# Kernel tuning notes

Measured on AMD Instinct MI355X. Metric: run time of the kernel, lower is better.

The kernel has to match this reference:

```python
import jax, jax.numpy as jnp
from jax import lax
import numpy as np

B, S, D_IN = 2048, 512, 5
H, E_DIM, N_EMB, C_CONV = 64, 32, 64, 32
COMMIT = 0.01


def _lstm_params(key, in_dim, hid):
    ks = jax.random.split(key, 4)
    sc = 1.0 / np.sqrt(hid)
    wih = jax.random.uniform(ks[0], (4 * hid, in_dim), minval=-sc, maxval=sc)
    whh = jax.random.uniform(ks[1], (4 * hid, hid), minval=-sc, maxval=sc)
    bih = jax.random.uniform(ks[2], (4 * hid,), minval=-sc, maxval=sc)
    bhh = jax.random.uniform(ks[3], (4 * hid,), minval=-sc, maxval=sc)
    return wih, whh, bih, bhh


def setup_inputs() -> dict:
    key = jax.random.key(0)
    ks = jax.random.split(key, 12)
    inp = {}
    inp['x'] = jax.random.normal(ks[0], (B, S, D_IN), dtype=jnp.float32)
    inp['conv_w'] = jax.random.normal(ks[1], (C_CONV, D_IN, 3)) * 0.2  # OIH
    inp['conv_b'] = jax.random.normal(ks[2], (C_CONV,)) * 0.05
    inp['bn_g'] = jnp.ones((C_CONV,)) + jax.random.normal(ks[3], (C_CONV,)) * 0.05
    inp['bn_b'] = jax.random.normal(ks[4], (C_CONV,)) * 0.05
    inp['bn_m'] = jax.random.normal(ks[5], (C_CONV,)) * 0.1
    inp['bn_v'] = jax.random.uniform(ks[6], (C_CONV,), minval=0.5, maxval=1.5)
    cw = _lstm_params(ks[7], C_CONV, H)
    cw1 = _lstm_params(jax.random.fold_in(ks[7], 1), H, H)
    vw = _lstm_params(ks[8], D_IN, H)
    vw1 = _lstm_params(jax.random.fold_in(ks[8], 1), H, H)
    for pre, p in (('cnn0', cw), ('cnn1', cw1), ('vq0', vw), ('vq1', vw1)):
        inp[pre + '_wih'], inp[pre + '_whh'], inp[pre + '_bih'], inp[pre + '_bhh'] = p
    inp['proj_w'] = jax.random.normal(ks[9], (E_DIM, H)) * (1.0 / np.sqrt(H))
    inp['proj_b'] = jax.random.normal(ks[10], (E_DIM,)) * 0.05
    xav = np.sqrt(6.0 / (N_EMB + E_DIM))
    inp['codebook'] = jax.random.uniform(ks[11], (N_EMB, E_DIM), minval=-xav, maxval=xav)
    return inp


def _lstm_layer(xs, wih, whh, bih, bhh):
    # xs: [S, B, in] -> (ys [S,B,H], h_final [B,H])
    b = xs.shape[1]
    h0 = jnp.zeros((b, H), xs.dtype)
    bias = bih + bhh

    def step(carry, x_t):
        h, c = carry
        gates = x_t @ wih.T + h @ whh.T + bias
        i, f, g, o = jnp.split(gates, 4, axis=-1)
        c = jax.nn.sigmoid(f) * c + jax.nn.sigmoid(i) * jnp.tanh(g)
        h = jax.nn.sigmoid(o) * jnp.tanh(c)
        return (h, c), h

    (h, c), ys = lax.scan(step, (h0, h0), xs)
    return ys, h


def _forward(x, conv_w, conv_b, bn_g, bn_b, bn_m, bn_v,
             cnn0_wih, cnn0_whh, cnn0_bih, cnn0_bhh,
             cnn1_wih, cnn1_whh, cnn1_bih, cnn1_bhh,
             vq0_wih, vq0_whh, vq0_bih, vq0_bhh,
             vq1_wih, vq1_whh, vq1_bih, vq1_bhh,
             proj_w, proj_b, codebook):
    # CNN stream: conv1d(k=3, pad=1) + BN (eval) + ReLU; dropout = identity (eval)
    x_ncw = jnp.transpose(x, (0, 2, 1))  # [B, D_IN, S]
    y = lax.conv_general_dilated(x_ncw, conv_w, (1,), [(1, 1)],
                                 dimension_numbers=('NCH', 'OIH', 'NCH'))
    y = y + conv_b[None, :, None]
    y = (y - bn_m[None, :, None]) * (bn_g / jnp.sqrt(bn_v + 1e-5))[None, :, None] + bn_b[None, :, None]
    y = jax.nn.relu(y)
    y = jnp.transpose(y, (2, 0, 1))  # [S, B, 32] time-major
    ys, _ = _lstm_layer(y, cnn0_wih, cnn0_whh, cnn0_bih, cnn0_bhh)
    _, cnn_features = _lstm_layer(ys, cnn1_wih, cnn1_whh, cnn1_bih, cnn1_bhh)  # [B, H]

    # VQ stream
    xt = jnp.transpose(x, (1, 0, 2))  # [S, B, D_IN]
    ys2, _ = _lstm_layer(xt, vq0_wih, vq0_whh, vq0_bih, vq0_bhh)
    _, vq_hidden = _lstm_layer(ys2, vq1_wih, vq1_whh, vq1_bih, vq1_bhh)  # [B, H]
    vq_proj = vq_hidden @ proj_w.T + proj_b  # [B, E_DIM]

    # Vector quantization
    d = (jnp.sum(vq_proj ** 2, axis=1, keepdims=True)
         + jnp.sum(codebook ** 2, axis=1)
         - 2.0 * vq_proj @ codebook.T)  # [B, N_EMB]
    idx = jnp.argmin(d, axis=1)
    quantized = codebook[idx]  # [B, E_DIM]
    e_loss = jnp.mean((lax.stop_gradient(quantized) - vq_proj) ** 2)
    q_loss = jnp.mean((quantized - lax.stop_gradient(vq_proj)) ** 2)
    vq_loss = q_loss + COMMIT * e_loss
    quantized = vq_proj + lax.stop_gradient(quantized - vq_proj)  # STE
    enc = jax.nn.one_hot(idx, N_EMB, dtype=vq_proj.dtype)
    avg_probs = jnp.mean(enc, axis=0)
    perplexity = jnp.exp(-jnp.sum(avg_probs * jnp.log(avg_probs + 1e-10)))

    combined = jnp.concatenate([cnn_features, quantized], axis=1)  # [B, H+E_DIM]
    return combined, vq_loss, perplexity


def reference(x, conv_w, conv_b, bn_g, bn_b, bn_m, bn_v,
              cnn0_wih, cnn0_whh, cnn0_bih, cnn0_bhh,
              cnn1_wih, cnn1_whh, cnn1_bih, cnn1_bhh,
              vq0_wih, vq0_whh, vq0_bih, vq0_bhh,
              vq1_wih, vq1_whh, vq1_bih, vq1_bhh,
              proj_w, proj_b, codebook):
    combined, vq_loss, perplexity = _forward(
        x, conv_w, conv_b, bn_g, bn_b, bn_m, bn_v,
        cnn0_wih, cnn0_whh, cnn0_bih, cnn0_bhh,
        cnn1_wih, cnn1_whh, cnn1_bih, cnn1_bhh,
        vq0_wih, vq0_whh, vq0_bih, vq0_bhh,
        vq1_wih, vq1_whh, vq1_bih, vq1_bhh,
        proj_w, proj_b, codebook)
    # num_classes=None -> returns (combined, combined, vq_loss, perplexity)
    return combined, combined, vq_loss, perplexity
```

## Files before the change

kernel.cpp:

```cpp
#include <hip/hip_runtime.h>
#include <math.h>
#include <stdint.h>

#define B_TOT 2048
#define SEQ   512
#define DIN   5
#define HID   64
#define EDIM  32
#define NEMB  64
#define BT    16
#define NBLK_STREAM 128
#define COMB  96
#define OUTC  (B_TOT*COMB)

typedef __attribute__((ext_vector_type(8))) _Float16 half8;
typedef __attribute__((ext_vector_type(4))) float float4v;

#if __has_builtin(__builtin_amdgcn_exp2f)
#define FEXP2(x) __builtin_amdgcn_exp2f(x)
#else
#define FEXP2(x) exp2f(x)
#endif
#if __has_builtin(__builtin_amdgcn_rcpf)
#define FRCP(x) __builtin_amdgcn_rcpf(x)
#else
#define FRCP(x) (1.0f/(x))
#endif

__device__ __forceinline__ float fsig(float x){
  return FRCP(1.0f + FEXP2(-1.44269504089f * x));
}
__device__ __forceinline__ float ftanh(float x){
  return fmaf(2.0f, FRCP(1.0f + FEXP2(-2.88539008178f * x)), -1.0f);
}
#define MFMA16(a,b,c) __builtin_amdgcn_mfma_f32_16x16x32_f16((a),(b),(c),0,0,0)

__global__ __launch_bounds__(1024)
__attribute__((amdgpu_waves_per_eu(4, 4)))
void fused_kernel(const float* __restrict__ xg,
                  const float* __restrict__ conv_w, const float* __restrict__ conv_b,
                  const float* __restrict__ bn_g, const float* __restrict__ bn_b,
                  const float* __restrict__ bn_m, const float* __restrict__ bn_v,
                  const float* __restrict__ cnn0_wih, const float* __restrict__ cnn0_whh,
                  const float* __restrict__ cnn0_bih, const float* __restrict__ cnn0_bhh,
                  const float* __restrict__ cnn1_wih, const float* __restrict__ cnn1_whh,
                  const float* __restrict__ cnn1_bih, const float* __restrict__ cnn1_bhh,
                  const float* __restrict__ vq0_wih, const float* __restrict__ vq0_whh,
                  const float* __restrict__ vq0_bih, const float* __restrict__ vq0_bhh,
                  const float* __restrict__ vq1_wih, const float* __restrict__ vq1_whh,
                  const float* __restrict__ vq1_bih, const float* __restrict__ vq1_bhh,
                  const float* __restrict__ proj_w, const float* __restrict__ proj_b,
                  const float* __restrict__ codebook,
                  float* __restrict__ out, float* __restrict__ ws_f,
                  int* __restrict__ ws_hist)
{
  __shared__ __align__(16) _Float16 ZT[2][5][4][BT][8];
  __shared__ __align__(16) float hfin[BT][HID];
  __shared__ __align__(16) float pbuf[BT][EDIM];
  __shared__ float xwin[4][BT][DIN];

  const int tid  = threadIdx.x;
  const bool is_cnn = (blockIdx.x < NBLK_STREAM);
  const int b0   = (is_cnn ? blockIdx.x : blockIdx.x - NBLK_STREAM) * BT;
  const int w    = tid >> 6;
  const int lane = tid & 63;
  const int n16  = lane & 15;
  const int quad = lane >> 4;
  const int u    = 4*w + quad;

  const float* wih0 = is_cnn ? cnn0_wih : vq0_wih;
  const float* whh0 = is_cnn ? cnn0_whh : vq0_whh;
  const float* bih0 = is_cnn ? cnn0_bih : vq0_bih;
  const float* bhh0 = is_cnn ? cnn0_bhh : vq0_bhh;
  const float* wih1 = is_cnn ? cnn1_wih : vq1_wih;
  const float* whh1 = is_cnn ? cnn1_whh : vq1_whh;
  const float* bih1 = is_cnn ? cnn1_bih : vq1_bih;
  const float* bhh1 = is_cnn ? cnn1_bhh : vq1_bhh;

  const int orow = 64*(n16 & 3) + 4*w + (n16 >> 2);
  half8 Ah0[3], Ah1[4];
#pragma unroll
  for (int kt = 0; kt < 3; ++kt) {
    half8 vh;
#pragma unroll
    for (int j = 0; j < 8; ++j) {
      const int g = kt*32 + quad*8 + j;
      float wv;
      if (is_cnn) wv = (g < 32) ? wih0[orow*32 + g] : whh0[orow*64 + (g-32)];
      else        wv = (g < 5) ? wih0[orow*5 + g] : (g < 32 ? 0.f : whh0[orow*64 + (g-32)]);
      vh[j] = (_Float16)wv;
    }
    Ah0[kt] = vh;
  }
#pragma unroll
  for (int kt = 0; kt < 4; ++kt) {
    half8 vh;
#pragma unroll
    for (int j = 0; j < 8; ++j) {
      const int g = kt*32 + quad*8 + j;
      float wv = (g < 64) ? wih1[orow*64 + g] : whh1[orow*64 + (g-64)];
      vh[j] = (_Float16)wv;
    }
    Ah1[kt] = vh;
  }

  float4v bc0, bc1;
#pragma unroll
  for (int r = 0; r < 4; ++r) {
    bc0[r] = bih0[64*r + u] + bhh0[64*r + u];
    bc1[r] = bih1[64*r + u] + bhh1[64*r + u];
  }

  float wr[16];
#pragma unroll
  for (int i = 0; i < 16; ++i) wr[i] = 0.f;
  if (is_cnn && tid < 512) {
    const int cc = tid >> 4;
    float s = bn_g[cc] * rsqrtf(bn_v[cc] + 1e-5f);
#pragma unroll
    for (int i = 0; i < 5; ++i)
#pragma unroll
      for (int tau = 0; tau < 3; ++tau)
        wr[tau*5 + i] = conv_w[cc*15 + i*3 + tau] * s;
    wr[15] = (conv_b[cc] - bn_m[cc]) * s + bn_b[cc];
  }

  for (int i2 = tid; i2 < 2*5*4*BT*8/2; i2 += 1024) ((uint32_t*)ZT)[i2] = 0;

  const int xn = tid / 5, xi = tid % 5;
  float xpref = 0.f;

  #define ZB(b) ((_Float16*)(&ZT[(b)][0][0][0][0]))
  #define ZIDX(tile,k32,n) (((tile)*4 + (((k32)>>3)&3))*(BT*8) + (n)*8 + ((k32)&7))

  if (is_cnn) {
    if (tid < BT*DIN) {
#pragma unroll
      for (int j = 0; j < 4; ++j)
        xwin[j][xn][xi] = xg[((size_t)(b0+xn)*SEQ + j)*DIN + xi];
    }
    __syncthreads();
    if (tid < 512) {
      const int cc = tid >> 4, cn = tid & 15;
      float s = wr[15];
#pragma unroll
      for (int i = 0; i < 5; ++i)
        s += wr[5+i]*xwin[0][cn][i] + wr[10+i]*xwin[1][cn][i];
      s = fmaxf(s, 0.f);
      ZB(1)[ZIDX(0, cc, cn)] = (_Float16)s;
    }
  } else {
    if (tid < BT*DIN) {
      float xv = xg[((size_t)(b0+xn)*SEQ + 0)*DIN + xi];
      ZB(1)[ZIDX(0, xi, xn)] = (_Float16)xv;
    }
  }
  __syncthreads();

  float c0 = 0.f, c1 = 0.f, h1v = 0.f;
  {
    half8 bt0 = *(const half8*)&ZT[1][0][quad][n16][0];
    half8 bt1 = *(const half8*)&ZT[1][1][quad][n16][0];
    half8 bt2 = *(const half8*)&ZT[1][2][quad][n16][0];
    float4v a0 = bc0;
    a0 = MFMA16(Ah0[0], bt0, a0);
    a0 = MFMA16(Ah0[1], bt1, a0);
    a0 = MFMA16(Ah0[2], bt2, a0);
    c0 = fsig(a0[1])*c0 + fsig(a0[0])*ftanh(a0[2]);
    float h0 = fsig(a0[3])*ftanh(c0);
    ZB(0)[ZIDX(1 + (u>>5), u & 31, n16)] = (_Float16)h0;
  }
  if (is_cnn) {
    if (tid < 512) {
      const int cc = tid >> 4, cn = tid & 15;
      float s = wr[15];
#pragma unroll
      for (int i = 0; i < 5; ++i)
        s += wr[i]*xwin[0][cn][i] + wr[5+i]*xwin[1][cn][i]
           + wr[10+i]*xwin[2][cn][i];
      s = fmaxf(s, 0.f);
      ZB(0)[ZIDX(0, cc, cn)] = (_Float16)s;
    }
    if (tid < BT*DIN) xpref = xg[((size_t)(b0+xn)*SEQ + 4)*DIN + xi];
  } else {
    if (tid < BT*DIN) {
      float xv = xg[((size_t)(b0+xn)*SEQ + 1)*DIN + xi];
      ZB(0)[ZIDX(0, xi, xn)] = (_Float16)xv;
      xpref = xg[((size_t)(b0+xn)*SEQ + 2)*DIN + xi];
    }
  }
  __syncthreads();

#pragma unroll 2
  for (int t = 0; t < SEQ; ++t) {
    const int rb = t & 1, wrb = rb ^ 1;
    half8 bt0 = *(const half8*)&ZT[rb][0][quad][n16][0];
    half8 bt1 = *(const half8*)&ZT[rb][1][quad][n16][0];
    half8 bt2 = *(const half8*)&ZT[rb][2][quad][n16][0];
    half8 bt3 = *(const half8*)&ZT[rb][3][quad][n16][0];
    half8 bt4 = *(const half8*)&ZT[rb][4][quad][n16][0];
    float4v a1 = bc1, a0 = bc0;
    a1 = MFMA16(Ah1[0], bt1, a1);
    a1 = MFMA16(Ah1[1], bt2, a1);
    a1 = MFMA16(Ah1[2], bt3, a1);
    a1 = MFMA16(Ah1[3], bt4, a1);
    a0 = MFMA16(Ah0[0], bt0, a0);
    a0 = MFMA16(Ah0[1], bt1, a0);
    a0 = MFMA16(Ah0[2], bt2, a0);

    {
      c1 = fsig(a1[1])*c1 + fsig(a1[0])*ftanh(a1[2]);
      float h1 = fsig(a1[3])*ftanh(c1);
      ZB(wrb)[ZIDX(3 + (u>>5), u & 31, n16)] = (_Float16)h1;
      if (is_cnn) h1v = h1;
      else if (t == SEQ-1) hfin[n16][u] = h1;
    }
    {
      c0 = fsig(a0[1])*c0 + fsig(a0[0])*ftanh(a0[2]);
      float h0 = fsig(a0[3])*ftanh(c0);
      ZB(wrb)[ZIDX(1 + (u>>5), u & 31, n16)] = (_Float16)h0;
    }
    if (is_cnn) {
      if (tid < 512) {
        const int cc = tid >> 4, cn = tid & 15;
        const int s1 = (t+1)&3, s2 = (t+2)&3, s3 = (t+3)&3;
        float s = wr[15];
#pragma unroll
        for (int i = 0; i < 5; ++i)
          s += wr[i]*xwin[s1][cn][i] + wr[5+i]*xwin[s2][cn][i]
             + wr[10+i]*xwin[s3][cn][i];
        s = fmaxf(s, 0.f);
        ZB(wrb)[ZIDX(0, cc, cn)] = (_Float16)s;
      }
      if (tid < BT*DIN) {
        xwin[t & 3][xn][xi] = xpref;
        const int tq = t + 5;
        xpref = (tq < SEQ) ? xg[((size_t)(b0+xn)*SEQ + tq)*DIN + xi] : 0.f;
      }
    } else {
      if (tid < BT*DIN) {
        ZB(wrb)[ZIDX(0, xi, xn)] = (_Float16)xpref;
        const int tq = t + 3;
        xpref = (tq < SEQ) ? xg[((size_t)(b0+xn)*SEQ + tq)*DIN + xi] : 0.f;
      }
    }
    __syncthreads();
  }

  if (is_cnn) {
    const size_t gb = (size_t)(b0 + n16);
    out[gb*COMB + u]        = h1v;
    out[OUTC + gb*COMB + u] = h1v;
  } else {
    if (tid < 512) {
      const int pn = tid >> 5, pe = tid & 31;
      float s = proj_b[pe];
      const float* pw = proj_w + pe*HID;
#pragma unroll
      for (int k = 0; k < HID; ++k) s += hfin[pn][k] * pw[k];
      pbuf[pn][pe] = s;
    }
    __syncthreads();
    {
      const int bb = w;
      const int nn = lane;
      const float* cbn = codebook + nn*EDIM;
      float d = 0.f;
#pragma unroll
      for (int k = 0; k < EDIM; ++k) { float df = pbuf[bb][k] - cbn[k]; d += df*df; }
      int bi = nn;
#pragma unroll
      for (int off = 32; off > 0; off >>= 1) {
        float od = __shfl_down(d, off, 64);
        int   oi = __shfl_down(bi, off, 64);
        if (od < d || (od == d && oi < bi)) { d = od; bi = oi; }
      }
      bi = __shfl(bi, 0, 64);
      float lv = 0.f;
      if (nn < EDIM) {
        float q = codebook[bi*EDIM + nn];
        const size_t gb = (size_t)(b0 + bb);
        out[gb*COMB + HID + nn]        = q;
        out[OUTC + gb*COMB + HID + nn] = q;
        float df = q - pbuf[bb][nn];
        lv = df*df;
      }
#pragma unroll
      for (int off = 32; off > 0; off >>= 1) lv += __shfl_down(lv, off, 64);
      if (nn == 0) { atomicAdd(ws_f, lv); atomicAdd(&ws_hist[bi], 1); }
    }
  }
}

__global__ void zero_ws_kernel(float* ws_f, int* ws_hist) {
  const int t = threadIdx.x;
  if (t == 0) ws_f[0] = 0.f;
  if (t < NEMB) ws_hist[t] = 0;
}

__global__ void vq_finalize_kernel(const float* __restrict__ ws_f,
                                   const int* __restrict__ ws_hist,
                                   float* __restrict__ out) {
  const int t = threadIdx.x;
  float p = (float)ws_hist[t] * (1.0f / (float)B_TOT);
  float e = -p * logf(p + 1e-10f);
#pragma unroll
  for (int off = 32; off > 0; off >>= 1) e += __shfl_down(e, off, 64);
  if (t == 0) {
    float mse = ws_f[0] * (1.0f / (float)(B_TOT * EDIM));
    out[2*OUTC + 0] = mse * 1.01f;
    out[2*OUTC + 1] = expf(e);
  }
}

extern "C" void kernel_launch(void* const* d_in, const int* in_sizes, int n_in,
                              void* d_out, int out_size, void* d_ws, size_t ws_size,
                              hipStream_t stream) {
  const float* x        = (const float*)d_in[0];
  const float* conv_w   = (const float*)d_in[1];
  const float* conv_b   = (const float*)d_in[2];
  const float* bn_g     = (const float*)d_in[3];
  const float* bn_b     = (const float*)d_in[4];
  const float* bn_m     = (const float*)d_in[5];
  const float* bn_v     = (const float*)d_in[6];
  const float* cnn0_wih = (const float*)d_in[7];
  const float* cnn0_whh = (const float*)d_in[8];
  const float* cnn0_bih = (const float*)d_in[9];
  const float* cnn0_bhh = (const float*)d_in[10];
  const float* cnn1_wih = (const float*)d_in[11];
  const float* cnn1_whh = (const float*)d_in[12];
  const float* cnn1_bih = (const float*)d_in[13];
  const float* cnn1_bhh = (const float*)d_in[14];
  const float* vq0_wih  = (const float*)d_in[15];
  const float* vq0_whh  = (const float*)d_in[16];
  const float* vq0_bih  = (const float*)d_in[17];
  const float* vq0_bhh  = (const float*)d_in[18];
  const float* vq1_wih  = (const float*)d_in[19];
  const float* vq1_whh  = (const float*)d_in[20];
  const float* vq1_bih  = (const float*)d_in[21];
  const float* vq1_bhh  = (const float*)d_in[22];
  const float* proj_w   = (const float*)d_in[23];
  const float* proj_b   = (const float*)d_in[24];
  const float* codebook = (const float*)d_in[25];

  float* out     = (float*)d_out;
  float* ws_f    = (float*)d_ws;
  int*   ws_hist = (int*)d_ws + 16;

  hipLaunchKernelGGL(zero_ws_kernel, dim3(1), dim3(64), 0, stream, ws_f, ws_hist);
  hipLaunchKernelGGL(fused_kernel, dim3(2*NBLK_STREAM), dim3(1024), 0, stream,
                     x, conv_w, conv_b, bn_g, bn_b, bn_m, bn_v,
                     cnn0_wih, cnn0_whh, cnn0_bih, cnn0_bhh,
                     cnn1_wih, cnn1_whh, cnn1_bih, cnn1_bhh,
                     vq0_wih, vq0_whh, vq0_bih, vq0_bhh,
                     vq1_wih, vq1_whh, vq1_bih, vq1_bhh,
                     proj_w, proj_b, codebook, out, ws_f, ws_hist);
  hipLaunchKernelGGL(vq_finalize_kernel, dim3(1), dim3(64), 0, stream, ws_f, ws_hist, out);
}
```

Measured before the change: 559.4 us.

## Precompute conv+BN+ReLU features into workspace and stream them into the LSTM loop

Adds a separate kernel that computes the folded conv/BN/ReLU features for all timesteps as fp16 into workspace. The CNN-stream LSTM blocks then load these prefetched half8 vectors instead of computing the convolution inside the serial time loop. The loop barrier is also replaced with an explicit lgkmcnt wait plus s_barrier. This takes per-step ALU work off the recurrent critical path, at the cost of an extra launch and about 64MB of global traffic. The new path is only taken when the workspace is large enough.

```diff
diff --git a/kernel.cpp b/kernel.cpp
--- a/kernel.cpp
+++ b/kernel.cpp
@@ -35,6 +35,57 @@
 }
 #define MFMA16(a,b,c) __builtin_amdgcn_mfma_f32_16x16x32_f16((a),(b),(c),0,0,0)
 
+#define LOOP_BARRIER() do { \
+    asm volatile("s_waitcnt lgkmcnt(0)" ::: "memory"); \
+    __builtin_amdgcn_s_barrier(); \
+  } while (0)
+
+__global__ __launch_bounds__(256)
+void conv_pre_kernel(const float* __restrict__ xg,
+                     const float* __restrict__ conv_w, const float* __restrict__ conv_b,
+                     const float* __restrict__ bn_g, const float* __restrict__ bn_b,
+                     const float* __restrict__ bn_m, const float* __restrict__ bn_v,
+                     _Float16* __restrict__ Y)
+{
+  __shared__ float wcs[16][32];
+  const int tid = threadIdx.x;
+  if (tid < 32) {
+    float s = bn_g[tid] * rsqrtf(bn_v[tid] + 1e-5f);
+#pragma unroll
+    for (int i = 0; i < 5; ++i)
+#pragma unroll
+      for (int tau = 0; tau < 3; ++tau)
+        wcs[tau*5 + i][tid] = conv_w[tid*15 + i*3 + tau] * s;
+    wcs[15][tid] = (conv_b[tid] - bn_m[tid]) * s + bn_b[tid];
+  }
+  __syncthreads();
+  const int total = B_TOT * SEQ;
+  for (int idx = blockIdx.x*256 + tid; idx < total; idx += gridDim.x*256) {
+    const int b = idx >> 9, t = idx & (SEQ-1);
+    const float* xb = xg + ((size_t)b*SEQ + t)*DIN;
+    float xm[5], x0[5], xp[5];
+#pragma unroll
+    for (int i = 0; i < 5; ++i) {
+      x0[i] = xb[i];
+      xm[i] = (t > 0)       ? xb[i - DIN] : 0.f;
+      xp[i] = (t < SEQ-1)   ? xb[i + DIN] : 0.f;
+    }
+    _Float16 yv[32];
+#pragma unroll
+    for (int ch = 0; ch < 32; ++ch) {
+      float s = wcs[15][ch];
+#pragma unroll
+      for (int i = 0; i < 5; ++i)
+        s += wcs[i][ch]*xm[i] + wcs[5+i][ch]*x0[i] + wcs[10+i][ch]*xp[i];
+      yv[ch] = (_Float16)fmaxf(s, 0.f);
+    }
+    half8* dst = (half8*)(Y + (size_t)idx*32);
+#pragma unroll
+    for (int g = 0; g < 4; ++g) dst[g] = *(half8*)&yv[g*8];
+  }
+}
+
+template<bool PRE>
 __global__ __launch_bounds__(1024)
 __attribute__((amdgpu_waves_per_eu(4, 4)))
 void fused_kernel(const float* __restrict__ xg,
@@ -50,7 +101,7 @@
                   const float* __restrict__ vq1_wih, const float* __restrict__ vq1_whh,
                   const float* __restrict__ vq1_bih, const float* __restrict__ vq1_bhh,
                   const float* __restrict__ proj_w, const float* __restrict__ proj_b,
-                  const float* __restrict__ codebook,
+                  const float* __restrict__ codebook, const _Float16* __restrict__ Yg,
                   float* __restrict__ out, float* __restrict__ ws_f,
                   int* __restrict__ ws_hist)
 {
@@ -112,47 +163,70 @@
   }
 
   float wr[16];
-#pragma unroll
-  for (int i = 0; i < 16; ++i) wr[i] = 0.f;
-  if (is_cnn && tid < 512) {
-    const int cc = tid >> 4;
-    float s = bn_g[cc] * rsqrtf(bn_v[cc] + 1e-5f);
-#pragma unroll
-    for (int i = 0; i < 5; ++i)
-#pragma unroll
-      for (int tau = 0; tau < 3; ++tau)
-        wr[tau*5 + i] = conv_w[cc*15 + i*3 + tau] * s;
-    wr[15] = (conv_b[cc] - bn_m[cc]) * s + bn_b[cc];
+  if (!PRE) {
+#pragma unroll
+    for (int i = 0; i < 16; ++i) wr[i] = 0.f;
+    if (is_cnn && tid < 512) {
+      const int cc = tid >> 4;
+      float s = bn_g[cc] * rsqrtf(bn_v[cc] + 1e-5f);
+#pragma unroll
+      for (int i = 0; i < 5; ++i)
+#pragma unroll
+        for (int tau = 0; tau < 3; ++tau)
+          wr[tau*5 + i] = conv_w[cc*15 + i*3 + tau] * s;
+      wr[15] = (conv_b[cc] - bn_m[cc]) * s + bn_b[cc];
+    }
   }
 
   for (int i2 = tid; i2 < 2*5*4*BT*8/2; i2 += 1024) ((uint32_t*)ZT)[i2] = 0;
 
   const int xn = tid / 5, xi = tid % 5;
+  const int yn = tid >> 2, ykg = tid & 3;
   float xpref = 0.f;
+  half8 ypref{};
+  const _Float16* Yb = nullptr;
+  if (PRE && is_cnn && tid < 64)
+    Yb = Yg + ((size_t)(b0 + yn)*SEQ)*32 + ykg*8;
 
   #define ZB(b) ((_Float16*)(&ZT[(b)][0][0][0][0]))
   #define ZIDX(tile,k32,n) (((tile)*4 + (((k32)>>3)&3))*(BT*8) + (n)*8 + ((k32)&7))
 
-  if (is_cnn) {
+  if (!PRE && is_cnn) {
     if (tid < BT*DIN) {
 #pragma unroll
       for (int j = 0; j < 4; ++j)
         xwin[j][xn][xi] = xg[((size_t)(b0+xn)*SEQ + j)*DIN + xi];
     }
-    __syncthreads();
-    if (tid < 512) {
-      const int cc = tid >> 4, cn = tid & 15;
-      float s = wr[15];
-#pragma unroll
-      for (int i = 0; i < 5; ++i)
-        s += wr[5+i]*xwin[0][cn][i] + wr[10+i]*xwin[1][cn][i];
-      s = fmaxf(s, 0.f);
-      ZB(1)[ZIDX(0, cc, cn)] = (_Float16)s;
+  }
+  __syncthreads();
+
+  if (is_cnn) {
+    if (PRE) {
+      if (tid < 64) {
+        half8 y0 = *(const half8*)(Yb + (size_t)0*32);
+        half8 y1 = *(const half8*)(Yb + (size_t)1*32);
+        ypref    = *(const half8*)(Yb + (size_t)2*32);
+        *(half8*)&ZB(1)[ykg*(BT*8) + yn*8] = y0;
+        *(half8*)&ZB(0)[ykg*(BT*8) + yn*8] = y1;
+      }
+    } else {
+      if (tid < 512) {
+        const int cc = tid >> 4, cn = tid & 15;
+        float s = wr[15];
+#pragma unroll
+        for (int i = 0; i < 5; ++i)
+          s += wr[5+i]*xwin[0][cn][i] + wr[10+i]*xwin[1][cn][i];
+        s = fmaxf(s, 0.f);
+        ZB(1)[ZIDX(0, cc, cn)] = (_Float16)s;
+      }
     }
   } else {
     if (tid < BT*DIN) {
-      float xv = xg[((size_t)(b0+xn)*SEQ + 0)*DIN + xi];
-      ZB(1)[ZIDX(0, xi, xn)] = (_Float16)xv;
+      float x0v = xg[((size_t)(b0+xn)*SEQ + 0)*DIN + xi];
+      float x1v = xg[((size_t)(b0+xn)*SEQ + 1)*DIN + xi];
+      ZB(1)[ZIDX(0, xi, xn)] = (_Float16)x0v;
+      ZB(0)[ZIDX(0, xi, xn)] = (_Float16)x1v;
+      xpref = xg[((size_t)(b0+xn)*SEQ + 2)*DIN + xi];
     }
   }
   __syncthreads();
@@ -170,7 +244,7 @@
     float h0 = fsig(a0[3])*ftanh(c0);
     ZB(0)[ZIDX(1 + (u>>5), u & 31, n16)] = (_Float16)h0;
   }
-  if (is_cnn) {
+  if (!PRE && is_cnn) {
     if (tid < 512) {
       const int cc = tid >> 4, cn = tid & 15;
       float s = wr[15];
@@ -182,12 +256,6 @@
       ZB(0)[ZIDX(0, cc, cn)] = (_Float16)s;
     }
     if (tid < BT*DIN) xpref = xg[((size_t)(b0+xn)*SEQ + 4)*DIN + xi];
-  } else {
-    if (tid < BT*DIN) {
-      float xv = xg[((size_t)(b0+xn)*SEQ + 1)*DIN + xi];
-      ZB(0)[ZIDX(0, xi, xn)] = (_Float16)xv;
-      xpref = xg[((size_t)(b0+xn)*SEQ + 2)*DIN + xi];
-    }
   }
   __syncthreads();
 
@@ -221,21 +289,29 @@
       ZB(wrb)[ZIDX(1 + (u>>5), u & 31, n16)] = (_Float16)h0;
     }
     if (is_cnn) {
-      if (tid < 512) {
-        const int cc = tid >> 4, cn = tid & 15;
-        const int s1 = (t+1)&3, s2 = (t+2)&3, s3 = (t+3)&3;
-        float s = wr[15];
-#pragma unroll
-        for (int i = 0; i < 5; ++i)
-          s += wr[i]*xwin[s1][cn][i] + wr[5+i]*xwin[s2][cn][i]
-             + wr[10+i]*xwin[s3][cn][i];
-        s = fmaxf(s, 0.f);
-        ZB(wrb)[ZIDX(0, cc, cn)] = (_Float16)s;
-      }
-      if (tid < BT*DIN) {
-        xwin[t & 3][xn][xi] = xpref;
-        const int tq = t + 5;
-        xpref = (tq < SEQ) ? xg[((size_t)(b0+xn)*SEQ + tq)*DIN + xi] : 0.f;
+      if (PRE) {
+        if (tid < 64) {
+          *(half8*)&ZB(wrb)[ykg*(BT*8) + yn*8] = ypref;
+          const int tq = t + 3;
+          if (tq < SEQ) ypref = *(const half8*)(Yb + (size_t)tq*32);
+        }
+      } else {
+        if (tid < 512) {
+          const int cc = tid >> 4, cn = tid & 15;
+          const int s1 = (t+1)&3, s2 = (t+2)&3, s3 = (t+3)&3;
+          float s = wr[15];
+#pragma unroll
+          for (int i = 0; i < 5; ++i)
+            s += wr[i]*xwin[s1][cn][i] + wr[5+i]*xwin[s2][cn][i]
+               + wr[10+i]*xwin[s3][cn][i];
+          s = fmaxf(s, 0.f);
+          ZB(wrb)[ZIDX(0, cc, cn)] = (_Float16)s;
+        }
+        if (tid < BT*DIN) {
+          xwin[t & 3][xn][xi] = xpref;
+          const int tq = t + 5;
+          xpref = (tq < SEQ) ? xg[((size_t)(b0+xn)*SEQ + tq)*DIN + xi] : 0.f;
+        }
       }
     } else {
       if (tid < BT*DIN) {
@@ -244,7 +320,7 @@
         xpref = (tq < SEQ) ? xg[((size_t)(b0+xn)*SEQ + tq)*DIN + xi] : 0.f;
       }
     }
-    __syncthreads();
+    LOOP_BARRIER();
   }
 
   if (is_cnn) {
@@ -347,13 +423,29 @@
   float* ws_f    = (float*)d_ws;
   int*   ws_hist = (int*)d_ws + 16;
 
+  const size_t Y_BYTES = (size_t)B_TOT * SEQ * 32 * sizeof(_Float16);
+  _Float16* Yg = (_Float16*)((char*)d_ws + 1024);
+  const bool use_pre = (ws_size >= 1024 + Y_BYTES);
+
   hipLaunchKernelGGL(zero_ws_kernel, dim3(1), dim3(64), 0, stream, ws_f, ws_hist);
-  hipLaunchKernelGGL(fused_kernel, dim3(2*NBLK_STREAM), dim3(1024), 0, stream,
-                     x, conv_w, conv_b, bn_g, bn_b, bn_m, bn_v,
-                     cnn0_wih, cnn0_whh, cnn0_bih, cnn0_bhh,
-                     cnn1_wih, cnn1_whh, cnn1_bih, cnn1_bhh,
-                     vq0_wih, vq0_whh, vq0_bih, vq0_bhh,
-                     vq1_wih, vq1_whh, vq1_bih, vq1_bhh,
-                     proj_w, proj_b, codebook, out, ws_f, ws_hist);
+  if (use_pre) {
+    hipLaunchKernelGGL(conv_pre_kernel, dim3(1024), dim3(256), 0, stream,
+                       x, conv_w, conv_b, bn_g, bn_b, bn_m, bn_v, Yg);
+    hipLaunchKernelGGL((fused_kernel<true>), dim3(2*NBLK_STREAM), dim3(1024), 0, stream,
+                       x, conv_w, conv_b, bn_g, bn_b, bn_m, bn_v,
+                       cnn0_wih, cnn0_whh, cnn0_bih, cnn0_bhh,
+                       cnn1_wih, cnn1_whh, cnn1_bih, cnn1_bhh,
+                       vq0_wih, vq0_whh, vq0_bih, vq0_bhh,
+                       vq1_wih, vq1_whh, vq1_bih, vq1_bhh,
+                       proj_w, proj_b, codebook, Yg, out, ws_f, ws_hist);
+  } else {
+    hipLaunchKernelGGL((fused_kernel<false>), dim3(2*NBLK_STREAM), dim3(1024), 0, stream,
+                       x, conv_w, conv_b, bn_g, bn_b, bn_m, bn_v,
+                       cnn0_wih, cnn0_whh, cnn0_bih, cnn0_bhh,
+                       cnn1_wih, cnn1_whh, cnn1_bih, cnn1_bhh,
+                       vq0_wih, vq0_whh, vq0_bih, vq0_bhh,
+                       vq1_wih, vq1_whh, vq1_bih, vq1_bhh,
+                       proj_w, proj_b, codebook, Yg, out, ws_f, ws_hist);
+  }
   hipLaunchKernelGGL(vq_finalize_kernel, dim3(1), dim3(64), 0, stream, ws_f, ws_hist, out);
 }
```

Result: slower. 609.5 us (+9.0%).
